# Kernel optimization log

Hardware: AMD Instinct MI355X
Metric: run time of the kernel (lower is better)

The kernel has to match this reference:

```python
import jax, jax.numpy as jnp
import numpy as np
from jax import lax

N_NODES = 32768   # 256 graphs x 128 nodes
N_GRAPHS = 256
DEG = 16          # fixed neighbor-list length per node
IN = 128
HID = 256
OUT = 16


def setup_inputs() -> dict:
    key = jax.random.key(0)
    ks = jax.random.split(key, 12)
    g = lambda k, s: jax.random.normal(k, s, dtype=jnp.float32) * 0.05
    return {
        "x": jax.random.normal(ks[0], (N_NODES, IN), dtype=jnp.float32),
        "neighbors": jax.random.randint(ks[1], (N_NODES, DEG), 0, N_NODES, dtype=jnp.int32),
        # conv1: LSTM(in=128, hid=128), fc_self/fc_neigh 128->256
        "Wi1": g(ks[2], (4 * IN, IN)),
        "Wh1": g(ks[3], (4 * IN, IN)),
        "bi1": jnp.zeros((4 * IN,), jnp.float32),
        "bh1": jnp.zeros((4 * IN,), jnp.float32),
        "Ws1": g(ks[4], (HID, IN)),
        "Wn1": g(ks[5], (HID, IN)),
        "b1": jnp.zeros((HID,), jnp.float32),
        # conv2: LSTM(in=256, hid=256), fc_self/fc_neigh 256->256
        "Wi2": g(ks[6], (4 * HID, HID)),
        "Wh2": g(ks[7], (4 * HID, HID)),
        "bi2": jnp.zeros((4 * HID,), jnp.float32),
        "bh2": jnp.zeros((4 * HID,), jnp.float32),
        "Ws2": g(ks[8], (HID, HID)),
        "Wn2": g(ks[9], (HID, HID)),
        "b2": jnp.zeros((HID,), jnp.float32),
        # classifier 256 -> 16
        "Wc": g(ks[10], (OUT, HID)),
        "bc": jnp.zeros((OUT,), jnp.float32),
    }


def _lstm_agg(h, neighbors, Wi, Wh, bi, bh):
    # DGL SAGEConv 'lstm' reducer: LSTM over each node's neighbor feature
    # sequence, hidden size == feature size; returns final hidden state.
    # h: [N, F], neighbors: [N, D]
    N, F = h.shape

    def step(carry, nbr_t):
        hs, cs = carry
        x = h[nbr_t]                                  # [N, F] gather
        gates = x @ Wi.T + hs @ Wh.T + (bi + bh)      # [N, 4F]
        i, f, g, o = jnp.split(gates, 4, axis=-1)     # PyTorch gate order
        c = jax.nn.sigmoid(f) * cs + jax.nn.sigmoid(i) * jnp.tanh(g)
        hn = jax.nn.sigmoid(o) * jnp.tanh(c)
        return (hn, c), None

    z = jnp.zeros((N, F), h.dtype)
    (hT, _), _ = lax.scan(step, (z, z), neighbors.T)  # scan over DEG steps
    return hT


def _sage_conv(h, neighbors, Wi, Wh, bi, bh, Ws, Wn, b):
    h_neigh = _lstm_agg(h, neighbors, Wi, Wh, bi, bh)
    return h @ Ws.T + h_neigh @ Wn.T + b


def reference(x, neighbors, Wi1, Wh1, bi1, bh1, Ws1, Wn1, b1,
              Wi2, Wh2, bi2, bh2, Ws2, Wn2, b2, Wc, bc):
    h = _sage_conv(x, neighbors, Wi1, Wh1, bi1, bh1, Ws1, Wn1, b1)
    h = jax.nn.relu(h)
    h = _sage_conv(h, neighbors, Wi2, Wh2, bi2, bh2, Ws2, Wn2, b2)
    h = jax.nn.relu(h)
    # dgl.mean_nodes over a batch of equal-size graphs
    hg = h.reshape(N_GRAPHS, N_NODES // N_GRAPHS, HID).mean(axis=1)  # [B, HID]
    return hg @ Wc.T + bc                                            # [B, OUT]
```

## Files before the change

kernel.cpp:

```cpp
#include <hip/hip_runtime.h>

#define N_NODES 32768
#define DEG 16
#define IN_F 128
#define HIDF 256
#define N_GRAPHS 256
#define NPG 128
#define OUT_F 16

typedef unsigned short u16;
typedef unsigned int u32;
typedef __bf16 bf16x8 __attribute__((ext_vector_type(8)));
typedef float f32x4 __attribute__((ext_vector_type(4)));
typedef u16 u16x4 __attribute__((ext_vector_type(4)));
typedef u16 u16x8 __attribute__((ext_vector_type(8)));

__device__ __forceinline__ u16 f2bf(float f) {
  union { float f; unsigned u; } v; v.f = f;
  return (u16)((v.u + 0x7FFFu + ((v.u >> 16) & 1u)) >> 16);
}
__device__ __forceinline__ float bf2f(u16 b) {
  union { unsigned u; float f; } v; v.u = ((unsigned)b) << 16;
  return v.f;
}
__device__ __forceinline__ float sigm(float x) { return 1.0f / (1.0f + __expf(-x)); }
__device__ __forceinline__ float tanhfast(float x) {
  float e = __expf(2.0f * x);
  return (e - 1.0f) / (e + 1.0f);
}


__global__ void k_prep_x(const float* __restrict__ x, u16* __restrict__ out, int n4) {
  int i = blockIdx.x * blockDim.x + threadIdx.x;
  if (i < n4) {
    float4 v = ((const float4*)x)[i];
    ushort4 o;
    o.x = f2bf(v.x); o.y = f2bf(v.y); o.z = f2bf(v.z); o.w = f2bf(v.w);
    ((ushort4*)out)[i] = o;
  }
}

__global__ void k_prep_wg(const float* __restrict__ Wi, const float* __restrict__ Wh,
                          const float* __restrict__ bi, const float* __restrict__ bh,
                          u16* __restrict__ Wip, u16* __restrict__ Whp,
                          float* __restrict__ bwp, int F) {
  int total = 4 * F * F;
  for (int idx = blockIdx.x * blockDim.x + threadIdx.x; idx < total;
       idx += gridDim.x * blockDim.x) {
    int p = idx / F, k = idx % F;
    int fe = p >> 2, g = p & 3;
    int orig = g * F + fe;
    Wip[idx] = f2bf(Wi[orig * F + k]);
    Whp[idx] = f2bf(Wh[orig * F + k]);
    if (k == 0) bwp[p] = bi[orig] + bh[orig];
  }
}

__global__ void k_prep_cast(const float* __restrict__ Ws, const float* __restrict__ Wn,
                            u16* __restrict__ Bs, u16* __restrict__ Bn, int n) {
  int i = blockIdx.x * blockDim.x + threadIdx.x;
  if (i < n) { Bs[i] = f2bf(Ws[i]); Bn[i] = f2bf(Wn[i]); }
}

template <int K, int NC>
__launch_bounds__(256, 4)
__global__ void k_gemm(const u16* __restrict__ A, const u16* __restrict__ B,
                       const float* __restrict__ bias, u16* __restrict__ C) {
  constexpr int ROWB = 2 * K;
  __shared__ u16 lds[64 * K];
  char* ldsb = (char*)lds;
  const int tid = threadIdx.x;
  const int w = tid >> 6;
  const int lane = tid & 63;
  const int l16 = lane & 15, lq = lane >> 4;
  const int row0 = blockIdx.x * 64;
  const int col0 = blockIdx.y * 128;

  constexpr int CH = K / 8;
  constexpr int RPI = 256 / CH;
#pragma unroll
  for (int it = 0; it < 64 / RPI; ++it) {
    int r = tid / CH + it * RPI;
    int ch = tid % CH;
    bf16x8 v = *(const bf16x8*)(A + (size_t)(row0 + r) * K + ch * 8);
    int bo = r * ROWB + ((ch * 16) ^ ((r & 7) << 4));
    *(bf16x8*)(ldsb + bo) = v;
  }
  __syncthreads();

  f32x4 acc[4][2];
#pragma unroll
  for (int mt = 0; mt < 4; ++mt)
#pragma unroll
    for (int nt = 0; nt < 2; ++nt)
#pragma unroll
      for (int j = 0; j < 4; ++j) acc[mt][nt][j] = 0.f;

  for (int ks = 0; ks < K / 32; ++ks) {
    bf16x8 a[4];
#pragma unroll
    for (int mt = 0; mt < 4; ++mt) {
      int r = mt * 16 + l16;
      int bo = r * ROWB + (((ks * 32 + lq * 8) * 2) ^ ((r & 7) << 4));
      a[mt] = *(const bf16x8*)(ldsb + bo);
    }
#pragma unroll
    for (int nt = 0; nt < 2; ++nt) {
      int coln = col0 + w * 32 + nt * 16 + l16;
      bf16x8 b = *(const bf16x8*)(B + (size_t)coln * K + ks * 32 + lq * 8);
#pragma unroll
      for (int mt = 0; mt < 4; ++mt)
        acc[mt][nt] = __builtin_amdgcn_mfma_f32_16x16x32_bf16(a[mt], b, acc[mt][nt], 0, 0, 0);
    }
  }
#pragma unroll
  for (int mt = 0; mt < 4; ++mt)
#pragma unroll
    for (int nt = 0; nt < 2; ++nt) {
      int coln = col0 + w * 32 + nt * 16 + l16;
      float bb = bias[coln];
#pragma unroll
      for (int j = 0; j < 4; ++j) {
        int r = row0 + mt * 16 + lq * 4 + j;
        C[(size_t)r * NC + coln] = f2bf(acc[mt][nt][j] + bb);
      }
    }
}

template <int K>
__launch_bounds__(256, 4)
__global__ void k_comb(const u16* __restrict__ A, const u16* __restrict__ B,
                       const u16* __restrict__ XS, u16* __restrict__ C) {
  constexpr int ROWB = 2 * K;
  __shared__ u16 lds[64 * K];
  char* ldsb = (char*)lds;
  const int tid = threadIdx.x;
  const int w = tid >> 6;
  const int lane = tid & 63;
  const int l16 = lane & 15, lq = lane >> 4;
  const int row0 = blockIdx.x * 64;
  const int col0 = blockIdx.y * 128;

  constexpr int CH = K / 8;
  constexpr int RPI = 256 / CH;
#pragma unroll
  for (int it = 0; it < 64 / RPI; ++it) {
    int r = tid / CH + it * RPI;
    int ch = tid % CH;
    bf16x8 v = *(const bf16x8*)(A + (size_t)(row0 + r) * K + ch * 8);
    int bo = r * ROWB + ((ch * 16) ^ ((r & 7) << 4));
    *(bf16x8*)(ldsb + bo) = v;
  }
  __syncthreads();

  f32x4 acc[4][2];
#pragma unroll
  for (int mt = 0; mt < 4; ++mt)
#pragma unroll
    for (int nt = 0; nt < 2; ++nt)
#pragma unroll
      for (int j = 0; j < 4; ++j) acc[mt][nt][j] = 0.f;

  for (int ks = 0; ks < K / 32; ++ks) {
    bf16x8 a[4];
#pragma unroll
    for (int mt = 0; mt < 4; ++mt) {
      int r = mt * 16 + l16;
      int bo = r * ROWB + (((ks * 32 + lq * 8) * 2) ^ ((r & 7) << 4));
      a[mt] = *(const bf16x8*)(ldsb + bo);
    }
#pragma unroll
    for (int nt = 0; nt < 2; ++nt) {
      int coln = col0 + w * 32 + nt * 16 + l16;
      bf16x8 b = *(const bf16x8*)(B + (size_t)coln * K + ks * 32 + lq * 8);
#pragma unroll
      for (int mt = 0; mt < 4; ++mt)
        acc[mt][nt] = __builtin_amdgcn_mfma_f32_16x16x32_bf16(a[mt], b, acc[mt][nt], 0, 0, 0);
    }
  }
#pragma unroll
  for (int mt = 0; mt < 4; ++mt)
#pragma unroll
    for (int nt = 0; nt < 2; ++nt) {
      int coln = col0 + w * 32 + nt * 16 + l16;
#pragma unroll
      for (int j = 0; j < 4; ++j) {
        int r = row0 + mt * 16 + lq * 4 + j;
        float v = acc[mt][nt][j] + bf2f(XS[(size_t)r * HIDF + coln]);
        C[(size_t)r * HIDF + coln] = f2bf(fmaxf(v, 0.f));
      }
    }
}

template <int F, bool T0>
__launch_bounds__(512, 8)
__global__ void k_step(const u16* __restrict__ hprev,
                       const u16* __restrict__ XW,
                       const u16* __restrict__ Whp,
                       const int* __restrict__ nbr,
                       int t,
                       u16* __restrict__ cT,
                       u16* __restrict__ hnext) {
  constexpr int ROWB = 2 * F;
  constexpr int KS = F / 32;
  constexpr int RBN = F / 16;
  __shared__ __align__(16) u16 Alds[64 * F];
  __shared__ __align__(16) u16 tl[128 * 24];
  char* ldsb = (char*)Alds;
  const int tid = threadIdx.x;
  const int w = tid >> 6;
  const int lane = tid & 63;
  const int l16 = lane & 15, lq = lane >> 4;

  const int p = blockIdx.x + RBN * blockIdx.y;
  const int s = p >> 3;
  const int rb = s % RBN;
  const int g = (p & 7) + 8 * (s / RBN);

  const int row0 = rb * 64;
  const int col0 = g * 128;
  const int feb = row0 >> 2;
  const int n = col0 + w * 16 + l16;

  const int nb = nbr[(size_t)n * DEG + t];

  if constexpr (!T0) {
    constexpr int CH = F / 8;
    constexpr int RPI = 512 / CH;
#pragma unroll
    for (int it = 0; it < 64 / RPI; ++it) {
      int r = tid / CH + it * RPI;
      int ch = tid % CH;
      bf16x8 v = *(const bf16x8*)(Whp + (size_t)(row0 + r) * F + ch * 8);
      int bo = r * ROWB + ((ch * 16) ^ ((r & 7) << 4));
      *(bf16x8*)(ldsb + bo) = v;
    }
  }

  u16x4 xw[4];
  float cold[4];
#pragma unroll
  for (int mt = 0; mt < 4; ++mt) {
    xw[mt] = *(const u16x4*)(XW + (size_t)nb * (4 * F) + row0 + mt * 16 + lq * 4);
    if constexpr (!T0)
      cold[mt] = bf2f(cT[(size_t)(feb + mt * 4 + lq) * N_NODES + n]);
  }

  f32x4 acc[4];
#pragma unroll
  for (int mt = 0; mt < 4; ++mt)
#pragma unroll
    for (int j = 0; j < 4; ++j) acc[mt][j] = 0.f;

  if constexpr (!T0) {
    __syncthreads();
    const u16* hb = hprev + (size_t)n * F + lq * 8;
#pragma unroll
    for (int ks = 0; ks < KS; ++ks) {
      bf16x8 b = *(const bf16x8*)(hb + ks * 32);
      bf16x8 a[4];
#pragma unroll
      for (int mt = 0; mt < 4; ++mt) {
        int r = mt * 16 + l16;
        int bo = r * ROWB + (((ks * 32 + lq * 8) * 2) ^ ((r & 7) << 4));
        a[mt] = *(const bf16x8*)(ldsb + bo);
      }
#pragma unroll
      for (int mt = 0; mt < 4; ++mt)
        acc[mt] = __builtin_amdgcn_mfma_f32_16x16x32_bf16(a[mt], b, acc[mt], 0, 0, 0);
    }
  }

#pragma unroll
  for (int mt = 0; mt < 4; ++mt) {
    int fe = feb + mt * 4 + lq;
    float pi = acc[mt][0] + bf2f(xw[mt][0]);
    float pf = acc[mt][1] + bf2f(xw[mt][1]);
    float pg = acc[mt][2] + bf2f(xw[mt][2]);
    float po = acc[mt][3] + bf2f(xw[mt][3]);
    float cn;
    if constexpr (T0) cn = sigm(pi) * tanhfast(pg);
    else              cn = sigm(pf) * cold[mt] + sigm(pi) * tanhfast(pg);
    float hn = sigm(po) * tanhfast(cn);
    cT[(size_t)fe * N_NODES + n] = f2bf(cn);
    tl[(w * 16 + l16) * 24 + mt * 4 + lq] = f2bf(hn);
  }
  __syncthreads();
  {
    int nloc = tid >> 2, q = tid & 3;
    u16x4 v = *(const u16x4*)&tl[nloc * 24 + q * 4];
    *(u16x4*)(hnext + (size_t)(col0 + nloc) * F + feb + q * 4) = v;
  }
}

__global__ void k_pool(const u16* __restrict__ h2, const float* __restrict__ Wc,
                       const float* __restrict__ bc, float* __restrict__ out) {
  __shared__ float hg[HIDF];
  int g = blockIdx.x;
  int tid = threadIdx.x;
  float s = 0.0f;
  for (int i = 0; i < NPG; ++i) s += bf2f(h2[(size_t)(g * NPG + i) * HIDF + tid]);
  hg[tid] = s * (1.0f / NPG);
  __syncthreads();
  if (tid < OUT_F) {
    float o = bc[tid];
    for (int fe = 0; fe < HIDF; ++fe) o += hg[fe] * Wc[tid * HIDF + fe];
    out[g * OUT_F + tid] = o;
  }
}

extern "C" void kernel_launch(void* const* d_in, const int* in_sizes, int n_in,
                              void* d_out, int out_size, void* d_ws, size_t ws_size,
                              hipStream_t stream) {
  const float* x   = (const float*)d_in[0];
  const int*   nbr = (const int*)d_in[1];
  const float* Wi1 = (const float*)d_in[2];
  const float* Wh1 = (const float*)d_in[3];
  const float* bi1 = (const float*)d_in[4];
  const float* bh1 = (const float*)d_in[5];
  const float* Ws1 = (const float*)d_in[6];
  const float* Wn1 = (const float*)d_in[7];
  const float* b1  = (const float*)d_in[8];
  const float* Wi2 = (const float*)d_in[9];
  const float* Wh2 = (const float*)d_in[10];
  const float* bi2 = (const float*)d_in[11];
  const float* bh2 = (const float*)d_in[12];
  const float* Ws2 = (const float*)d_in[13];
  const float* Wn2 = (const float*)d_in[14];
  const float* b2  = (const float*)d_in[15];
  const float* Wc  = (const float*)d_in[16];
  const float* bc  = (const float*)d_in[17];
  float* out = (float*)d_out;

  char* ws = (char*)d_ws;
  const size_t MB = 1u << 20;
  u16*   x16 = (u16*)(ws + 0);
  u16*   XW1 = (u16*)(ws + 8 * MB);
  u16*   XS1 = (u16*)(ws + 40 * MB);
  u16*   X2  = XS1;
  u16*   hA1 = (u16*)(ws + 56 * MB);
  u16*   hB1 = (u16*)(ws + 64 * MB);
  u16*   c1  = (u16*)(ws + 72 * MB);
  u16*   XW2 = (u16*)(ws + 80 * MB);
  u16*   XS2 = (u16*)(ws + 0);
  u16*   h2o = XS2;
  u16*   hA2 = (u16*)(ws + 16 * MB);
  u16*   hB2 = (u16*)(ws + 32 * MB);
  u16*   c2  = (u16*)(ws + 56 * MB);
  char* wr = ws + 144 * MB;
  size_t off = 0;
  auto alloc = [&](size_t bytes) { void* p = wr + off; off += (bytes + 255) & ~(size_t)255; return p; };
  u16*   Wip1 = (u16*)alloc(512 * 128 * 2);
  u16*   Whp1 = (u16*)alloc(512 * 128 * 2);
  float* bwp1 = (float*)alloc(512 * 4);
  u16*   Bs1  = (u16*)alloc(256 * 128 * 2);
  u16*   Bn1  = (u16*)alloc(256 * 128 * 2);
  u16*   Wip2 = (u16*)alloc(1024 * 256 * 2);
  u16*   Whp2 = (u16*)alloc(1024 * 256 * 2);
  float* bwp2 = (float*)alloc(1024 * 4);
  u16*   Bs2  = (u16*)alloc(256 * 256 * 2);
  u16*   Bn2  = (u16*)alloc(256 * 256 * 2);

  k_prep_x<<<dim3(N_NODES * IN_F / 4 / 256), dim3(256), 0, stream>>>(x, x16, N_NODES * IN_F / 4);
  k_prep_wg<<<dim3(256), dim3(256), 0, stream>>>(Wi1, Wh1, bi1, bh1, Wip1, Whp1, bwp1, IN_F);
  k_prep_wg<<<dim3(1024), dim3(256), 0, stream>>>(Wi2, Wh2, bi2, bh2, Wip2, Whp2, bwp2, HIDF);
  k_prep_cast<<<dim3(128), dim3(256), 0, stream>>>(Ws1, Wn1, Bs1, Bn1, 256 * 128);
  k_prep_cast<<<dim3(256), dim3(256), 0, stream>>>(Ws2, Wn2, Bs2, Bn2, 256 * 256);

  k_gemm<128, 512><<<dim3(N_NODES / 64, 4), dim3(256), 0, stream>>>(x16, Wip1, bwp1, XW1);
  k_gemm<128, 256><<<dim3(N_NODES / 64, 2), dim3(256), 0, stream>>>(x16, Bs1, b1, XS1);
  {
    k_step<IN_F, true><<<dim3(8, N_NODES / 128), dim3(512), 0, stream>>>(
        hA1, XW1, Whp1, nbr, 0, c1, hA1);
    u16* hc = hA1; u16* hn = hB1;
    for (int t = 1; t < DEG; ++t) {
      k_step<IN_F, false><<<dim3(8, N_NODES / 128), dim3(512), 0, stream>>>(
          hc, XW1, Whp1, nbr, t, c1, hn);
      u16* tmp = hc; hc = hn; hn = tmp;
    }
    k_comb<128><<<dim3(N_NODES / 64, 2), dim3(256), 0, stream>>>(hc, Bn1, XS1, X2);
  }

  k_gemm<256, 1024><<<dim3(N_NODES / 64, 8), dim3(256), 0, stream>>>(X2, Wip2, bwp2, XW2);
  k_gemm<256, 256><<<dim3(N_NODES / 64, 2), dim3(256), 0, stream>>>(X2, Bs2, b2, XS2);
  {
    k_step<HIDF, true><<<dim3(16, N_NODES / 128), dim3(512), 0, stream>>>(
        hA2, XW2, Whp2, nbr, 0, c2, hA2);
    u16* hc = hA2; u16* hn = hB2;
    for (int t = 1; t < DEG; ++t) {
      k_step<HIDF, false><<<dim3(16, N_NODES / 128), dim3(512), 0, stream>>>(
          hc, XW2, Whp2, nbr, t, c2, hn);
      u16* tmp = hc; hc = hn; hn = tmp;
    }
    k_comb<256><<<dim3(N_NODES / 64, 2), dim3(256), 0, stream>>>(hc, Bn2, XS2, h2o);
  }

  k_pool<<<dim3(N_GRAPHS), dim3(256), 0, stream>>>(h2o, Wc, bc, out);
}
```

Measured before the change: 1.385 ms.

## Double node tile per LSTM step block and permute Wi for vectorized XW loads

Each k_step block now handles 256 nodes instead of 128, with every wave computing two 16-node MFMA tiles. This reuses the LDS-staged Wh tile across twice as many nodes and halves the number of blocks that reload it. The Wi gate permutation in prep is reordered so each lane can load its precomputed input projection as two 16-byte vectors instead of four 8-byte loads, and the h output is written in wider 16-byte chunks. The cost is more registers per thread (launch bounds occupancy hint lowered from 8 to 4), a larger LDS transpose buffer, and half as many blocks in flight.

```diff
diff --git a/kernel.cpp b/kernel.cpp
--- a/kernel.cpp
+++ b/kernel.cpp
@@ -48,11 +48,20 @@
   for (int idx = blockIdx.x * blockDim.x + threadIdx.x; idx < total;
        idx += gridDim.x * blockDim.x) {
     int p = idx / F, k = idx % F;
-    int fe = p >> 2, g = p & 3;
-    int orig = g * F + fe;
-    Wip[idx] = f2bf(Wi[orig * F + k]);
-    Whp[idx] = f2bf(Wh[orig * F + k]);
-    if (k == 0) bwp[p] = bi[orig] + bh[orig];
+    {
+      int fe = p >> 2, g = p & 3;
+      int orig = g * F + fe;
+      Whp[idx] = f2bf(Wh[orig * F + k]);
+    }
+    {
+      int base = p & ~63, local = p & 63;
+      int lq = local >> 4, mt = (local >> 2) & 3, gate = local & 3;
+      int oldp = base + mt * 16 + lq * 4 + gate;
+      int fe = oldp >> 2, g = oldp & 3;
+      int orig = g * F + fe;
+      Wip[idx] = f2bf(Wi[orig * F + k]);
+      if (k == 0) bwp[p] = bi[orig] + bh[orig];
+    }
   }
 }
 
@@ -193,7 +202,7 @@
 }
 
 template <int F, bool T0>
-__launch_bounds__(512, 8)
+__launch_bounds__(512, 4)
 __global__ void k_step(const u16* __restrict__ hprev,
                        const u16* __restrict__ XW,
                        const u16* __restrict__ Whp,
@@ -205,7 +214,7 @@
   constexpr int KS = F / 32;
   constexpr int RBN = F / 16;
   __shared__ __align__(16) u16 Alds[64 * F];
-  __shared__ __align__(16) u16 tl[128 * 24];
+  __shared__ __align__(16) u16 tl[256 * 24];
   char* ldsb = (char*)Alds;
   const int tid = threadIdx.x;
   const int w = tid >> 6;
@@ -218,11 +227,13 @@
   const int g = (p & 7) + 8 * (s / RBN);
 
   const int row0 = rb * 64;
-  const int col0 = g * 128;
+  const int col0 = g * 256;
   const int feb = row0 >> 2;
-  const int n = col0 + w * 16 + l16;
-
-  const int nb = nbr[(size_t)n * DEG + t];
+  const int n0 = col0 + w * 32 + l16;
+  const int n1 = n0 + 16;
+
+  const int nb0 = nbr[(size_t)n0 * DEG + t];
+  const int nb1 = nbr[(size_t)n1 * DEG + t];
 
   if constexpr (!T0) {
     constexpr int CH = F / 8;
@@ -237,27 +248,41 @@
     }
   }
 
-  u16x4 xw[4];
-  float cold[4];
-#pragma unroll
-  for (int mt = 0; mt < 4; ++mt) {
-    xw[mt] = *(const u16x4*)(XW + (size_t)nb * (4 * F) + row0 + mt * 16 + lq * 4);
-    if constexpr (!T0)
-      cold[mt] = bf2f(cT[(size_t)(feb + mt * 4 + lq) * N_NODES + n]);
-  }
-
-  f32x4 acc[4];
+  u16x8 xwv[2][2];
+  {
+    const u16* b0 = XW + (size_t)nb0 * (4 * F) + row0 + lq * 16;
+    const u16* b1 = XW + (size_t)nb1 * (4 * F) + row0 + lq * 16;
+    xwv[0][0] = *(const u16x8*)(b0);
+    xwv[0][1] = *(const u16x8*)(b0 + 8);
+    xwv[1][0] = *(const u16x8*)(b1);
+    xwv[1][1] = *(const u16x8*)(b1 + 8);
+  }
+
+  float cold[4][2];
+  if constexpr (!T0) {
+#pragma unroll
+    for (int mt = 0; mt < 4; ++mt) {
+      cold[mt][0] = bf2f(cT[(size_t)(feb + mt * 4 + lq) * N_NODES + n0]);
+      cold[mt][1] = bf2f(cT[(size_t)(feb + mt * 4 + lq) * N_NODES + n1]);
+    }
+  }
+
+  f32x4 acc[4][2];
 #pragma unroll
   for (int mt = 0; mt < 4; ++mt)
 #pragma unroll
-    for (int j = 0; j < 4; ++j) acc[mt][j] = 0.f;
+    for (int nt = 0; nt < 2; ++nt)
+#pragma unroll
+      for (int j = 0; j < 4; ++j) acc[mt][nt][j] = 0.f;
 
   if constexpr (!T0) {
     __syncthreads();
-    const u16* hb = hprev + (size_t)n * F + lq * 8;
+    const u16* hb0 = hprev + (size_t)n0 * F + lq * 8;
+    const u16* hb1 = hprev + (size_t)n1 * F + lq * 8;
 #pragma unroll
     for (int ks = 0; ks < KS; ++ks) {
-      bf16x8 b = *(const bf16x8*)(hb + ks * 32);
+      bf16x8 b0 = *(const bf16x8*)(hb0 + ks * 32);
+      bf16x8 b1 = *(const bf16x8*)(hb1 + ks * 32);
       bf16x8 a[4];
 #pragma unroll
       for (int mt = 0; mt < 4; ++mt) {
@@ -266,30 +291,44 @@
         a[mt] = *(const bf16x8*)(ldsb + bo);
       }
 #pragma unroll
-      for (int mt = 0; mt < 4; ++mt)
-        acc[mt] = __builtin_amdgcn_mfma_f32_16x16x32_bf16(a[mt], b, acc[mt], 0, 0, 0);
+      for (int mt = 0; mt < 4; ++mt) {
+        acc[mt][0] = __builtin_amdgcn_mfma_f32_16x16x32_bf16(a[mt], b0, acc[mt][0], 0, 0, 0);
+        acc[mt][1] = __builtin_amdgcn_mfma_f32_16x16x32_bf16(a[mt], b1, acc[mt][1], 0, 0, 0);
+      }
     }
   }
 
 #pragma unroll
   for (int mt = 0; mt < 4; ++mt) {
     int fe = feb + mt * 4 + lq;
-    float pi = acc[mt][0] + bf2f(xw[mt][0]);
-    float pf = acc[mt][1] + bf2f(xw[mt][1]);
-    float pg = acc[mt][2] + bf2f(xw[mt][2]);
-    float po = acc[mt][3] + bf2f(xw[mt][3]);
-    float cn;
-    if constexpr (T0) cn = sigm(pi) * tanhfast(pg);
-    else              cn = sigm(pf) * cold[mt] + sigm(pi) * tanhfast(pg);
-    float hn = sigm(po) * tanhfast(cn);
-    cT[(size_t)fe * N_NODES + n] = f2bf(cn);
-    tl[(w * 16 + l16) * 24 + mt * 4 + lq] = f2bf(hn);
+#pragma unroll
+    for (int nt = 0; nt < 2; ++nt) {
+      int n = nt ? n1 : n0;
+      float pi, pf, pg, po;
+      if (mt < 2) {
+        pi = acc[mt][nt][0] + bf2f(xwv[nt][0][(mt & 1) * 4 + 0]);
+        pf = acc[mt][nt][1] + bf2f(xwv[nt][0][(mt & 1) * 4 + 1]);
+        pg = acc[mt][nt][2] + bf2f(xwv[nt][0][(mt & 1) * 4 + 2]);
+        po = acc[mt][nt][3] + bf2f(xwv[nt][0][(mt & 1) * 4 + 3]);
+      } else {
+        pi = acc[mt][nt][0] + bf2f(xwv[nt][1][(mt & 1) * 4 + 0]);
+        pf = acc[mt][nt][1] + bf2f(xwv[nt][1][(mt & 1) * 4 + 1]);
+        pg = acc[mt][nt][2] + bf2f(xwv[nt][1][(mt & 1) * 4 + 2]);
+        po = acc[mt][nt][3] + bf2f(xwv[nt][1][(mt & 1) * 4 + 3]);
+      }
+      float cn;
+      if constexpr (T0) cn = sigm(pi) * tanhfast(pg);
+      else              cn = sigm(pf) * cold[mt][nt] + sigm(pi) * tanhfast(pg);
+      float hn = sigm(po) * tanhfast(cn);
+      cT[(size_t)fe * N_NODES + n] = f2bf(cn);
+      tl[(w * 32 + nt * 16 + l16) * 24 + mt * 4 + lq] = f2bf(hn);
+    }
   }
   __syncthreads();
   {
-    int nloc = tid >> 2, q = tid & 3;
-    u16x4 v = *(const u16x4*)&tl[nloc * 24 + q * 4];
-    *(u16x4*)(hnext + (size_t)(col0 + nloc) * F + feb + q * 4) = v;
+    int nloc = tid >> 1, q = tid & 1;
+    u16x8 v = *(const u16x8*)&tl[nloc * 24 + q * 8];
+    *(u16x8*)(hnext + (size_t)(col0 + nloc) * F + feb + q * 8) = v;
   }
 }
 
@@ -370,11 +409,11 @@
   k_gemm<128, 512><<<dim3(N_NODES / 64, 4), dim3(256), 0, stream>>>(x16, Wip1, bwp1, XW1);
   k_gemm<128, 256><<<dim3(N_NODES / 64, 2), dim3(256), 0, stream>>>(x16, Bs1, b1, XS1);
   {
-    k_step<IN_F, true><<<dim3(8, N_NODES / 128), dim3(512), 0, stream>>>(
+    k_step<IN_F, true><<<dim3(8, N_NODES / 256), dim3(512), 0, stream>>>(
         hA1, XW1, Whp1, nbr, 0, c1, hA1);
     u16* hc = hA1; u16* hn = hB1;
     for (int t = 1; t < DEG; ++t) {
-      k_step<IN_F, false><<<dim3(8, N_NODES / 128), dim3(512), 0, stream>>>(
+      k_step<IN_F, false><<<dim3(8, N_NODES / 256), dim3(512), 0, stream>>>(
           hc, XW1, Whp1, nbr, t, c1, hn);
       u16* tmp = hc; hc = hn; hn = tmp;
     }
@@ -384,11 +423,11 @@
   k_gemm<256, 1024><<<dim3(N_NODES / 64, 8), dim3(256), 0, stream>>>(X2, Wip2, bwp2, XW2);
   k_gemm<256, 256><<<dim3(N_NODES / 64, 2), dim3(256), 0, stream>>>(X2, Bs2, b2, XS2);
   {
-    k_step<HIDF, true><<<dim3(16, N_NODES / 128), dim3(512), 0, stream>>>(
+    k_step<HIDF, true><<<dim3(16, N_NODES / 256), dim3(512), 0, stream>>>(
         hA2, XW2, Whp2, nbr, 0, c2, hA2);
     u16* hc = hA2; u16* hn = hB2;
     for (int t = 1; t < DEG; ++t) {
-      k_step<HIDF, false><<<dim3(16, N_NODES / 128), dim3(512), 0, stream>>>(
+      k_step<HIDF, false><<<dim3(16, N_NODES / 256), dim3(512), 0, stream>>>(
           hc, XW2, Whp2, nbr, t, c2, hn);
       u16* tmp = hc; hc = hn; hn = tmp;
     }
```

After: 1.284 ms, median of 2. 1.08x faster.
